# Kernel tuning notes

Measured on AMD Instinct MI355X. Metric: run time of the kernel, lower is better.

The kernel has to match this reference:

```python
import jax, jax.numpy as jnp
import numpy as np

EMB = 2048
HEADS = 16
HEAD_DIM = EMB // HEADS
LATENT = 512
B, S = 2, 2048


def setup_inputs() -> dict:
    key = jax.random.key(0)
    ks = jax.random.split(key, 7)
    sc = lambda fan_in: 1.0 / np.sqrt(fan_in)
    return {
        "x": jax.random.normal(ks[0], (B, S, EMB), dtype=jnp.float32),
        "w_q": jax.random.normal(ks[1], (EMB, EMB), dtype=jnp.float32) * sc(EMB),
        "w_down": jax.random.normal(ks[2], (LATENT, EMB), dtype=jnp.float32) * sc(EMB),
        "w_up_k": jax.random.normal(ks[3], (EMB, LATENT), dtype=jnp.float32) * sc(LATENT),
        "w_up_v": jax.random.normal(ks[4], (EMB, LATENT), dtype=jnp.float32) * sc(LATENT),
        "w_out": jax.random.normal(ks[5], (EMB, EMB), dtype=jnp.float32) * sc(EMB),
        "b_out": jax.random.normal(ks[6], (EMB,), dtype=jnp.float32) * 0.01,
    }


def reference(x, w_q, w_down, w_up_k, w_up_v, w_out, b_out):
    # Linear uses torch convention: y = x @ W.T
    q = jnp.einsum("bse,fe->bsf", x, w_q)          # [B,S,EMB]
    latent = jnp.einsum("bse,le->bsl", x, w_down)  # [B,S,LATENT]
    k = jnp.einsum("bsl,fl->bsf", latent, w_up_k)
    v = jnp.einsum("bsl,fl->bsf", latent, w_up_v)

    def heads(t):  # [B,S,EMB] -> [B,H,S,D]
        return t.reshape(B, S, HEADS, HEAD_DIM).transpose(0, 2, 1, 3)

    qh, kh, vh = heads(q), heads(k), heads(v)
    scores = jnp.einsum("bhqd,bhkd->bhqk", qh, kh)  # [B,H,S,S]
    qpos = jnp.arange(S)
    causal = qpos[:, None] < qpos[None, :]          # True where future (masked)
    scores = jnp.where(causal[None, None], -jnp.inf, scores)
    attn = jax.nn.softmax(scores / np.sqrt(HEAD_DIM).astype(np.float32), axis=-1)
    ctx = jnp.einsum("bhqk,bhkd->bhqd", attn, vh)   # [B,H,S,D]
    ctx = ctx.transpose(0, 2, 1, 3).reshape(B, S, EMB)
    return jnp.einsum("bse,fe->bsf", ctx, w_out) + b_out
```

## Files before the change

kernel.cpp:

```cpp
#include <hip/hip_runtime.h>
#include <hip/hip_bf16.h>

#define EMB 2048
#define HEADS 16
#define HDIM 128
#define LATENT 512
#define BATCH 2
#define SEQ 2048
#define MROWS (BATCH*SEQ)

typedef __attribute__((ext_vector_type(4))) float f32x4;
typedef __attribute__((ext_vector_type(8))) short s16x8;

__device__ __forceinline__ unsigned short f2bf(float f) {
  __hip_bfloat16 h = __float2bfloat16(f);
  union { __hip_bfloat16 h; unsigned short u; } c; c.h = h; return c.u;
}

#define GLOAD_LDS16(g, l) \
  __builtin_amdgcn_global_load_lds((const __attribute__((address_space(1))) unsigned int*)(g), \
                                   (__attribute__((address_space(3))) unsigned int*)(l), 16, 0, 0)

__global__ void cvt_kernel(const float* __restrict__ src, unsigned short* __restrict__ dst, int n4) {
  int i = blockIdx.x * blockDim.x + threadIdx.x;
  int stride = gridDim.x * blockDim.x;
  for (; i < n4; i += stride) {
    float4 v = reinterpret_cast<const float4*>(src)[i];
    ushort4 o;
    o.x = f2bf(v.x); o.y = f2bf(v.y); o.z = f2bf(v.z); o.w = f2bf(v.w);
    reinterpret_cast<ushort4*>(dst)[i] = o;
  }
}

#define BM 128
#define BN 128
#define BK 32

template<int OUTF32>
__global__ __launch_bounds__(256) void gemm_bt(
    const unsigned short* __restrict__ A, const unsigned short* __restrict__ B,
    void* __restrict__ C, const float* __restrict__ bias, int M, int N, int K)
{
  __shared__ __align__(16) unsigned short sA[BM][BK];
  __shared__ __align__(16) unsigned short sB[BN][BK];
  const int tid  = threadIdx.x;
  const int lane = tid & 63, wave = tid >> 6;
  const int wm = wave >> 1, wn = wave & 1;
  const int lrow = lane & 15, kgrp = lane >> 4;
  const long bm = (long)blockIdx.y * BM, bn = (long)blockIdx.x * BN;
  const int srow = tid >> 2;
  const int scol = (tid & 3) * 8;

  f32x4 zero4 = {0.f, 0.f, 0.f, 0.f};
  f32x4 acc[4][4];
  #pragma unroll
  for (int i = 0; i < 4; ++i)
    #pragma unroll
    for (int j = 0; j < 4; ++j) acc[i][j] = zero4;

  const unsigned short* ga = A + (bm + srow) * (long)K + scol;
  const unsigned short* gb = B + (bn + srow) * (long)K + scol;

  for (int k0 = 0; k0 < K; k0 += BK) {
    GLOAD_LDS16(ga + k0,                 &sA[srow][scol]);
    GLOAD_LDS16(ga + 64*(long)K + k0,    &sA[srow + 64][scol]);
    GLOAD_LDS16(gb + k0,                 &sB[srow][scol]);
    GLOAD_LDS16(gb + 64*(long)K + k0,    &sB[srow + 64][scol]);
    __syncthreads();

    s16x8 aF[4], bF[4];
    #pragma unroll
    for (int i = 0; i < 4; ++i) {
      aF[i] = *reinterpret_cast<const s16x8*>(&sA[wm*64 + i*16 + lrow][kgrp*8]);
      bF[i] = *reinterpret_cast<const s16x8*>(&sB[wn*64 + i*16 + lrow][kgrp*8]);
    }
    #pragma unroll
    for (int i = 0; i < 4; ++i)
      #pragma unroll
      for (int j = 0; j < 4; ++j)
        acc[i][j] = __builtin_amdgcn_mfma_f32_16x16x32_bf16(aF[i], bF[j], acc[i][j], 0, 0, 0);
    __syncthreads();
  }

  #pragma unroll
  for (int i = 0; i < 4; ++i) {
    #pragma unroll
    for (int j = 0; j < 4; ++j) {
      long row = bm + wm*64 + i*16 + kgrp*4;
      long col = bn + wn*64 + j*16 + lrow;
      if (OUTF32) {
        float* Cf = (float*)C;
        float bv = bias[col];
        #pragma unroll
        for (int r = 0; r < 4; ++r) Cf[(row + r) * (long)N + col] = acc[i][j][r] + bv;
      } else {
        unsigned short* Cb = (unsigned short*)C;
        #pragma unroll
        for (int r = 0; r < 4; ++r) Cb[(row + r) * (long)N + col] = f2bf(acc[i][j][r]);
      }
    }
  }
}

#define KVB 64
#define QTILE 128
#define NQT (SEQ/QTILE)

__global__ __launch_bounds__(256, 1) void attn2_kernel(
    const unsigned short* __restrict__ Q, const unsigned short* __restrict__ Kg,
    const unsigned short* __restrict__ Vt, unsigned short* __restrict__ CTX)
{
  const int b = blockIdx.z, h = blockIdx.y, pr = blockIdx.x;
  const int tid = threadIdx.x, w = tid >> 6, lane = tid & 63;
  const int lrow = lane & 15, kgrp = lane >> 4;
  const size_t bS = (size_t)b * SEQ;

  __shared__ __align__(16) unsigned short sK[2][KVB * HDIM];
  __shared__ __align__(16) unsigned short sP[4][32][72];

  const int krow  = tid >> 4;
  const int kcolB = ((tid & 15) * 16) ^ (((tid >> 4) & 7) << 4);
  const unsigned short* kst_g = Kg + (bS + krow) * EMB + h * HDIM + (kcolB >> 1);

  const int swz = (lrow & 7) << 4;
  int cc[4];
  #pragma unroll
  for (int kk = 0; kk < 4; ++kk) cc[kk] = ((kk * 64 + kgrp * 16) ^ swz) >> 1;

  const float C = 0.12751742f;
  f32x4 zero4 = {0.f, 0.f, 0.f, 0.f};

  const int qts[2] = {NQT - 1 - pr, pr};
  for (int ps = 0; ps < 2; ++ps) {
    const int qt = qts[ps];
    const int nt = 2 * qt + 2;
    const int qw = qt * QTILE + w * 32;

    s16x8 qF[2][4];
    #pragma unroll
    for (int g = 0; g < 2; ++g)
      #pragma unroll
      for (int kk = 0; kk < 4; ++kk)
        qF[g][kk] = *reinterpret_cast<const s16x8*>(
            Q + (bS + qw + g * 16 + lrow) * EMB + h * HDIM + kk * 32 + kgrp * 8);

    f32x4 o[2][8];
    float rm[2][4], rl[2][4];
    #pragma unroll
    for (int g = 0; g < 2; ++g) {
      #pragma unroll
      for (int dt = 0; dt < 8; ++dt) o[g][dt] = zero4;
      #pragma unroll
      for (int r = 0; r < 4; ++r) { rm[g][r] = -1.0e30f; rl[g][r] = 0.f; }
    }

    __syncthreads();
    {
      unsigned short* l0 = &sK[0][0] + tid * 8;
      #pragma unroll
      for (int R = 0; R < 4; ++R) GLOAD_LDS16(kst_g + (size_t)R * 16 * EMB, l0 + R * 2048);
    }

    for (int j = 0; j < nt; ++j) {
      __syncthreads();
      const int kv0 = j * KVB;
      if (j + 1 < nt) {
        const unsigned short* gs = kst_g + (size_t)(j + 1) * KVB * EMB;
        unsigned short* ls = &sK[(j + 1) & 1][0] + tid * 8;
        #pragma unroll
        for (int R = 0; R < 4; ++R) GLOAD_LDS16(gs + (size_t)R * 16 * EMB, ls + R * 2048);
      }

      s16x8 vF[2][8];
      #pragma unroll
      for (int hf = 0; hf < 2; ++hf)
        #pragma unroll
        for (int dt = 0; dt < 8; ++dt)
          vF[hf][dt] = *reinterpret_cast<const s16x8*>(
              Vt + (size_t)(h * HDIM + dt * 16 + lrow) * MROWS + bS + kv0 + hf * 32 + kgrp * 8);

      const unsigned short* kb = &sK[j & 1][0];
      f32x4 sc[2][4];
      #pragma unroll
      for (int g = 0; g < 2; ++g)
        #pragma unroll
        for (int kvg = 0; kvg < 4; ++kvg) sc[g][kvg] = zero4;
      #pragma unroll
      for (int kvg = 0; kvg < 4; ++kvg) {
        const int rb = (kvg * 16 + lrow) * HDIM;
        #pragma unroll
        for (int kk = 0; kk < 4; ++kk) {
          s16x8 kF = *reinterpret_cast<const s16x8*>(kb + rb + cc[kk]);
          sc[0][kvg] = __builtin_amdgcn_mfma_f32_16x16x32_bf16(qF[0][kk], kF, sc[0][kvg], 0, 0, 0);
          sc[1][kvg] = __builtin_amdgcn_mfma_f32_16x16x32_bf16(qF[1][kk], kF, sc[1][kvg], 0, 0, 0);
        }
      }

      #pragma unroll
      for (int g = 0; g < 2; ++g) {
        const bool needm = (kv0 + 63 > qw + g * 16);
        float sv[4][4];
        #pragma unroll
        for (int kvg = 0; kvg < 4; ++kvg)
          #pragma unroll
          for (int r = 0; r < 4; ++r) {
            float s = sc[g][kvg][r];
            if (needm) {
              int qq  = qw + g * 16 + kgrp * 4 + r;
              int col = kv0 + kvg * 16 + lrow;
              s = (col <= qq) ? s : -3.0e38f;
            }
            sv[kvg][r] = s;
          }
        float tm[4];
        #pragma unroll
        for (int r = 0; r < 4; ++r)
          tm[r] = fmaxf(fmaxf(sv[0][r], sv[1][r]), fmaxf(sv[2][r], sv[3][r]));
        #pragma unroll
        for (int m = 1; m < 16; m <<= 1)
          #pragma unroll
          for (int r = 0; r < 4; ++r) tm[r] = fmaxf(tm[r], __shfl_xor(tm[r], m));

        float corr[4], ts[4];
        #pragma unroll
        for (int r = 0; r < 4; ++r) {
          float mn = fmaxf(rm[g][r], tm[r] * C);
          corr[r] = exp2f(rm[g][r] - mn);
          rm[g][r] = mn;
          float p0 = exp2f(fmaf(sv[0][r], C, -mn));
          float p1 = exp2f(fmaf(sv[1][r], C, -mn));
          float p2 = exp2f(fmaf(sv[2][r], C, -mn));
          float p3 = exp2f(fmaf(sv[3][r], C, -mn));
          ts[r] = (p0 + p1) + (p2 + p3);
          const int qrow = g * 16 + kgrp * 4 + r;
          sP[w][qrow][ 0 + lrow] = f2bf(p0);
          sP[w][qrow][16 + lrow] = f2bf(p1);
          sP[w][qrow][32 + lrow] = f2bf(p2);
          sP[w][qrow][48 + lrow] = f2bf(p3);
        }
        #pragma unroll
        for (int m = 1; m < 16; m <<= 1)
          #pragma unroll
          for (int r = 0; r < 4; ++r) ts[r] += __shfl_xor(ts[r], m);
        #pragma unroll
        for (int r = 0; r < 4; ++r) rl[g][r] = rl[g][r] * corr[r] + ts[r];
        #pragma unroll
        for (int dt = 0; dt < 8; ++dt)
          #pragma unroll
          for (int r = 0; r < 4; ++r) o[g][dt][r] *= corr[r];
      }

      s16x8 pF[2][2];
      #pragma unroll
      for (int g = 0; g < 2; ++g)
        #pragma unroll
        for (int hf = 0; hf < 2; ++hf)
          pF[g][hf] = *reinterpret_cast<const s16x8*>(&sP[w][g * 16 + lrow][hf * 32 + kgrp * 8]);
      #pragma unroll
      for (int g = 0; g < 2; ++g)
        #pragma unroll
        for (int dt = 0; dt < 8; ++dt) {
          o[g][dt] = __builtin_amdgcn_mfma_f32_16x16x32_bf16(pF[g][0], vF[0][dt], o[g][dt], 0, 0, 0);
          o[g][dt] = __builtin_amdgcn_mfma_f32_16x16x32_bf16(pF[g][1], vF[1][dt], o[g][dt], 0, 0, 0);
        }
    }

    #pragma unroll
    for (int g = 0; g < 2; ++g) {
      float iv[4];
      #pragma unroll
      for (int r = 0; r < 4; ++r) iv[r] = 1.0f / rl[g][r];
      #pragma unroll
      for (int dt = 0; dt < 8; ++dt)
        #pragma unroll
        for (int r = 0; r < 4; ++r)
          CTX[(bS + qw + g * 16 + kgrp * 4 + r) * EMB + h * HDIM + dt * 16 + lrow] =
              f2bf(o[g][dt][r] * iv[r]);
    }
  }
}

extern "C" void kernel_launch(void* const* d_in, const int* in_sizes, int n_in,
                              void* d_out, int out_size, void* d_ws, size_t ws_size,
                              hipStream_t stream)
{
  const float* x      = (const float*)d_in[0];
  const float* w_q    = (const float*)d_in[1];
  const float* w_down = (const float*)d_in[2];
  const float* w_upk  = (const float*)d_in[3];
  const float* w_upv  = (const float*)d_in[4];
  const float* w_out  = (const float*)d_in[5];
  const float* b_out  = (const float*)d_in[6];
  float* out = (float*)d_out;

  char* ws = (char*)d_ws;
  size_t off = 0;
  auto alloc = [&](size_t elems) {
    void* p = ws + off; off += elems * 2; off = (off + 255) & ~(size_t)255; return p;
  };
  unsigned short* xb   = (unsigned short*)alloc((size_t)MROWS * EMB);
  unsigned short* wqb  = (unsigned short*)alloc((size_t)EMB * EMB);
  unsigned short* wdb  = (unsigned short*)alloc((size_t)LATENT * EMB);
  unsigned short* wkb  = (unsigned short*)alloc((size_t)EMB * LATENT);
  unsigned short* wvb  = (unsigned short*)alloc((size_t)EMB * LATENT);
  unsigned short* wob  = (unsigned short*)alloc((size_t)EMB * EMB);
  unsigned short* qb   = (unsigned short*)alloc((size_t)MROWS * EMB);
  unsigned short* latb = (unsigned short*)alloc((size_t)MROWS * LATENT);
  unsigned short* kb   = (unsigned short*)alloc((size_t)MROWS * EMB);
  unsigned short* vtb  = (unsigned short*)alloc((size_t)EMB * MROWS);
  unsigned short* ctxb = xb;

  auto cvt = [&](const float* s, unsigned short* d, size_t n) {
    int n4 = (int)(n / 4);
    int blocks = (n4 + 255) / 256; if (blocks > 1024) blocks = 1024;
    cvt_kernel<<<dim3(blocks), dim3(256), 0, stream>>>(s, d, n4);
  };
  cvt(x,      xb,  (size_t)MROWS * EMB);
  cvt(w_q,    wqb, (size_t)EMB * EMB);
  cvt(w_down, wdb, (size_t)LATENT * EMB);
  cvt(w_upk,  wkb, (size_t)EMB * LATENT);
  cvt(w_upv,  wvb, (size_t)EMB * LATENT);
  cvt(w_out,  wob, (size_t)EMB * EMB);

  gemm_bt<0><<<dim3(EMB/BN,    MROWS/BM), 256, 0, stream>>>(xb,   wqb, qb,   nullptr, MROWS, EMB,    EMB);
  gemm_bt<0><<<dim3(LATENT/BN, MROWS/BM), 256, 0, stream>>>(xb,   wdb, latb, nullptr, MROWS, LATENT, EMB);
  gemm_bt<0><<<dim3(EMB/BN,    MROWS/BM), 256, 0, stream>>>(latb, wkb, kb,   nullptr, MROWS, EMB,    LATENT);
  gemm_bt<0><<<dim3(MROWS/BN,  EMB/BM),   256, 0, stream>>>(wvb,  latb, vtb, nullptr, EMB,   MROWS,  LATENT);

  attn2_kernel<<<dim3(NQT/2, HEADS, BATCH), 256, 0, stream>>>(qb, kb, vtb, ctxb);

  gemm_bt<1><<<dim3(EMB/BN, MROWS/BM), 256, 0, stream>>>(ctxb, wob, (void*)out, b_out, MROWS, EMB, EMB);
}
```

Baseline: 465.1 us.

## Shrink attention query tile, add lazy softmax rescale, setprio, and GEMM block swizzle

The attention kernel now uses 64-row query tiles with 16 rows per wave, halving register use so two blocks can fit per CU, and launches twice as many blocks. It skips the running-max rescale of the output accumulator when the new max exceeds the old one by no more than a threshold. It also raises wave priority around the MFMA sections. Separately, the GEMM remaps block indices so consecutive workgroups are spread across eight groups, aimed at better cache locality across XCDs. The smaller tile loads each K/V tile for fewer query rows, so global and LDS traffic per unit of work goes up.

```diff
diff --git a/kernel.cpp b/kernel.cpp
--- a/kernel.cpp
+++ b/kernel.cpp
@@ -47,7 +47,14 @@
   const int lane = tid & 63, wave = tid >> 6;
   const int wm = wave >> 1, wn = wave & 1;
   const int lrow = lane & 15, kgrp = lane >> 4;
-  const long bm = (long)blockIdx.y * BM, bn = (long)blockIdx.x * BN;
+
+  const int gx = gridDim.x;
+  const int nwg = gx * gridDim.y;
+  const int orig = blockIdx.y * gx + blockIdx.x;
+  const int chunk = nwg >> 3;
+  const int sw = (orig & 7) * chunk + (orig >> 3);
+  const long bm = (long)(sw / gx) * BM, bn = (long)(sw % gx) * BN;
+
   const int srow = tid >> 2;
   const int scol = (tid & 3) * 8;
 
@@ -103,20 +110,20 @@
 }
 
 #define KVB 64
-#define QTILE 128
-#define NQT (SEQ/QTILE)
-
-__global__ __launch_bounds__(256, 1) void attn2_kernel(
+#define QTB 64
+#define NQT3 (SEQ/QTB)
+
+__global__ __launch_bounds__(256, 2) void attn3_kernel(
     const unsigned short* __restrict__ Q, const unsigned short* __restrict__ Kg,
     const unsigned short* __restrict__ Vt, unsigned short* __restrict__ CTX)
 {
-  const int b = blockIdx.z, h = blockIdx.y, pr = blockIdx.x;
+  const int pr = blockIdx.x, h = blockIdx.y, b = blockIdx.z;
   const int tid = threadIdx.x, w = tid >> 6, lane = tid & 63;
   const int lrow = lane & 15, kgrp = lane >> 4;
   const size_t bS = (size_t)b * SEQ;
 
   __shared__ __align__(16) unsigned short sK[2][KVB * HDIM];
-  __shared__ __align__(16) unsigned short sP[4][32][72];
+  __shared__ __align__(16) unsigned short sP[4][16][72];
 
   const int krow  = tid >> 4;
   const int kcolB = ((tid & 15) * 16) ^ (((tid >> 4) & 7) << 4);
@@ -128,31 +135,27 @@
   for (int kk = 0; kk < 4; ++kk) cc[kk] = ((kk * 64 + kgrp * 16) ^ swz) >> 1;
 
   const float C = 0.12751742f;
+  const float THR = 11.5f;
   f32x4 zero4 = {0.f, 0.f, 0.f, 0.f};
 
-  const int qts[2] = {NQT - 1 - pr, pr};
+  const int qts[2] = {NQT3 - 1 - pr, pr};
   for (int ps = 0; ps < 2; ++ps) {
     const int qt = qts[ps];
-    const int nt = 2 * qt + 2;
-    const int qw = qt * QTILE + w * 32;
-
-    s16x8 qF[2][4];
-    #pragma unroll
-    for (int g = 0; g < 2; ++g)
-      #pragma unroll
-      for (int kk = 0; kk < 4; ++kk)
-        qF[g][kk] = *reinterpret_cast<const s16x8*>(
-            Q + (bS + qw + g * 16 + lrow) * EMB + h * HDIM + kk * 32 + kgrp * 8);
-
-    f32x4 o[2][8];
-    float rm[2][4], rl[2][4];
-    #pragma unroll
-    for (int g = 0; g < 2; ++g) {
-      #pragma unroll
-      for (int dt = 0; dt < 8; ++dt) o[g][dt] = zero4;
-      #pragma unroll
-      for (int r = 0; r < 4; ++r) { rm[g][r] = -1.0e30f; rl[g][r] = 0.f; }
-    }
+    const int nt = qt + 1;
+    const int qw = qt * QTB + w * 16;
+
+    s16x8 qF[4];
+    #pragma unroll
+    for (int kk = 0; kk < 4; ++kk)
+      qF[kk] = *reinterpret_cast<const s16x8*>(
+          Q + (bS + qw + lrow) * EMB + h * HDIM + kk * 32 + kgrp * 8);
+
+    f32x4 o[8];
+    #pragma unroll
+    for (int dt = 0; dt < 8; ++dt) o[dt] = zero4;
+    float rm[4], rl[4];
+    #pragma unroll
+    for (int r = 0; r < 4; ++r) { rm[r] = -1.0e30f; rl[r] = 0.f; }
 
     __syncthreads();
     {
@@ -180,103 +183,111 @@
               Vt + (size_t)(h * HDIM + dt * 16 + lrow) * MROWS + bS + kv0 + hf * 32 + kgrp * 8);
 
       const unsigned short* kb = &sK[j & 1][0];
-      f32x4 sc[2][4];
-      #pragma unroll
-      for (int g = 0; g < 2; ++g)
-        #pragma unroll
-        for (int kvg = 0; kvg < 4; ++kvg) sc[g][kvg] = zero4;
+      f32x4 sc[4];
+      #pragma unroll
+      for (int kvg = 0; kvg < 4; ++kvg) sc[kvg] = zero4;
+      __builtin_amdgcn_s_setprio(1);
       #pragma unroll
       for (int kvg = 0; kvg < 4; ++kvg) {
         const int rb = (kvg * 16 + lrow) * HDIM;
         #pragma unroll
         for (int kk = 0; kk < 4; ++kk) {
           s16x8 kF = *reinterpret_cast<const s16x8*>(kb + rb + cc[kk]);
-          sc[0][kvg] = __builtin_amdgcn_mfma_f32_16x16x32_bf16(qF[0][kk], kF, sc[0][kvg], 0, 0, 0);
-          sc[1][kvg] = __builtin_amdgcn_mfma_f32_16x16x32_bf16(qF[1][kk], kF, sc[1][kvg], 0, 0, 0);
+          sc[kvg] = __builtin_amdgcn_mfma_f32_16x16x32_bf16(qF[kk], kF, sc[kvg], 0, 0, 0);
         }
       }
-
-      #pragma unroll
-      for (int g = 0; g < 2; ++g) {
-        const bool needm = (kv0 + 63 > qw + g * 16);
-        float sv[4][4];
-        #pragma unroll
-        for (int kvg = 0; kvg < 4; ++kvg)
-          #pragma unroll
-          for (int r = 0; r < 4; ++r) {
-            float s = sc[g][kvg][r];
-            if (needm) {
-              int qq  = qw + g * 16 + kgrp * 4 + r;
-              int col = kv0 + kvg * 16 + lrow;
-              s = (col <= qq) ? s : -3.0e38f;
-            }
-            sv[kvg][r] = s;
+      __builtin_amdgcn_s_setprio(0);
+
+      const bool needm = (kv0 + 63 > qw);
+      float sv[4][4];
+      #pragma unroll
+      for (int kvg = 0; kvg < 4; ++kvg)
+        #pragma unroll
+        for (int r = 0; r < 4; ++r) {
+          float s = sc[kvg][r];
+          if (needm) {
+            int qq  = qw + kgrp * 4 + r;
+            int col = kv0 + kvg * 16 + lrow;
+            s = (col <= qq) ? s : -3.0e38f;
           }
-        float tm[4];
-        #pragma unroll
-        for (int r = 0; r < 4; ++r)
-          tm[r] = fmaxf(fmaxf(sv[0][r], sv[1][r]), fmaxf(sv[2][r], sv[3][r]));
-        #pragma unroll
-        for (int m = 1; m < 16; m <<= 1)
-          #pragma unroll
-          for (int r = 0; r < 4; ++r) tm[r] = fmaxf(tm[r], __shfl_xor(tm[r], m));
-
-        float corr[4], ts[4];
+          sv[kvg][r] = s;
+        }
+      float tm[4];
+      #pragma unroll
+      for (int r = 0; r < 4; ++r)
+        tm[r] = fmaxf(fmaxf(sv[0][r], sv[1][r]), fmaxf(sv[2][r], sv[3][r]));
+      #pragma unroll
+      for (int m = 1; m < 16; m <<= 1)
+        #pragma unroll
+        for (int r = 0; r < 4; ++r) tm[r] = fmaxf(tm[r], __shfl_xor(tm[r], m));
+
+      float d = tm[0] * C - rm[0];
+      #pragma unroll
+      for (int r = 1; r < 4; ++r) d = fmaxf(d, tm[r] * C - rm[r]);
+      const bool skip = __all(d <= THR);
+
+      float mn[4];
+      #pragma unroll
+      for (int r = 0; r < 4; ++r) mn[r] = skip ? rm[r] : fmaxf(rm[r], tm[r] * C);
+
+      float ts[4];
+      #pragma unroll
+      for (int r = 0; r < 4; ++r) {
+        float p0 = exp2f(fmaf(sv[0][r], C, -mn[r]));
+        float p1 = exp2f(fmaf(sv[1][r], C, -mn[r]));
+        float p2 = exp2f(fmaf(sv[2][r], C, -mn[r]));
+        float p3 = exp2f(fmaf(sv[3][r], C, -mn[r]));
+        ts[r] = (p0 + p1) + (p2 + p3);
+        const int qrow = kgrp * 4 + r;
+        sP[w][qrow][ 0 + lrow] = f2bf(p0);
+        sP[w][qrow][16 + lrow] = f2bf(p1);
+        sP[w][qrow][32 + lrow] = f2bf(p2);
+        sP[w][qrow][48 + lrow] = f2bf(p3);
+      }
+      #pragma unroll
+      for (int m = 1; m < 16; m <<= 1)
+        #pragma unroll
+        for (int r = 0; r < 4; ++r) ts[r] += __shfl_xor(ts[r], m);
+
+      if (skip) {
+        #pragma unroll
+        for (int r = 0; r < 4; ++r) rl[r] += ts[r];
+      } else {
+        float corr[4];
         #pragma unroll
         for (int r = 0; r < 4; ++r) {
-          float mn = fmaxf(rm[g][r], tm[r] * C);
-          corr[r] = exp2f(rm[g][r] - mn);
-          rm[g][r] = mn;
-          float p0 = exp2f(fmaf(sv[0][r], C, -mn));
-          float p1 = exp2f(fmaf(sv[1][r], C, -mn));
-          float p2 = exp2f(fmaf(sv[2][r], C, -mn));
-          float p3 = exp2f(fmaf(sv[3][r], C, -mn));
-          ts[r] = (p0 + p1) + (p2 + p3);
-          const int qrow = g * 16 + kgrp * 4 + r;
-          sP[w][qrow][ 0 + lrow] = f2bf(p0);
-          sP[w][qrow][16 + lrow] = f2bf(p1);
-          sP[w][qrow][32 + lrow] = f2bf(p2);
-          sP[w][qrow][48 + lrow] = f2bf(p3);
+          corr[r] = exp2f(rm[r] - mn[r]);
+          rm[r] = mn[r];
+          rl[r] = rl[r] * corr[r] + ts[r];
         }
-        #pragma unroll
-        for (int m = 1; m < 16; m <<= 1)
-          #pragma unroll
-          for (int r = 0; r < 4; ++r) ts[r] += __shfl_xor(ts[r], m);
-        #pragma unroll
-        for (int r = 0; r < 4; ++r) rl[g][r] = rl[g][r] * corr[r] + ts[r];
         #pragma unroll
         for (int dt = 0; dt < 8; ++dt)
           #pragma unroll
-          for (int r = 0; r < 4; ++r) o[g][dt][r] *= corr[r];
-      }
-
-      s16x8 pF[2][2];
-      #pragma unroll
-      for (int g = 0; g < 2; ++g)
-        #pragma unroll
-        for (int hf = 0; hf < 2; ++hf)
-          pF[g][hf] = *reinterpret_cast<const s16x8*>(&sP[w][g * 16 + lrow][hf * 32 + kgrp * 8]);
-      #pragma unroll
-      for (int g = 0; g < 2; ++g)
-        #pragma unroll
-        for (int dt = 0; dt < 8; ++dt) {
-          o[g][dt] = __builtin_amdgcn_mfma_f32_16x16x32_bf16(pF[g][0], vF[0][dt], o[g][dt], 0, 0, 0);
-          o[g][dt] = __builtin_amdgcn_mfma_f32_16x16x32_bf16(pF[g][1], vF[1][dt], o[g][dt], 0, 0, 0);
-        }
+          for (int r = 0; r < 4; ++r) o[dt][r] *= corr[r];
+      }
+
+      s16x8 pF[2];
+      #pragma unroll
+      for (int hf = 0; hf < 2; ++hf)
+        pF[hf] = *reinterpret_cast<const s16x8*>(&sP[w][lrow][hf * 32 + kgrp * 8]);
+      __builtin_amdgcn_s_setprio(1);
+      #pragma unroll
+      for (int dt = 0; dt < 8; ++dt) {
+        o[dt] = __builtin_amdgcn_mfma_f32_16x16x32_bf16(pF[0], vF[0][dt], o[dt], 0, 0, 0);
+        o[dt] = __builtin_amdgcn_mfma_f32_16x16x32_bf16(pF[1], vF[1][dt], o[dt], 0, 0, 0);
+      }
+      __builtin_amdgcn_s_setprio(0);
     }
 
-    #pragma unroll
-    for (int g = 0; g < 2; ++g) {
-      float iv[4];
-      #pragma unroll
-      for (int r = 0; r < 4; ++r) iv[r] = 1.0f / rl[g][r];
-      #pragma unroll
-      for (int dt = 0; dt < 8; ++dt)
-        #pragma unroll
-        for (int r = 0; r < 4; ++r)
-          CTX[(bS + qw + g * 16 + kgrp * 4 + r) * EMB + h * HDIM + dt * 16 + lrow] =
-              f2bf(o[g][dt][r] * iv[r]);
-    }
+    float iv[4];
+    #pragma unroll
+    for (int r = 0; r < 4; ++r) iv[r] = 1.0f / rl[r];
+    #pragma unroll
+    for (int dt = 0; dt < 8; ++dt)
+      #pragma unroll
+      for (int r = 0; r < 4; ++r)
+        CTX[(bS + qw + kgrp * 4 + r) * EMB + h * HDIM + dt * 16 + lrow] =
+            f2bf(o[dt][r] * iv[r]);
   }
 }
 
@@ -327,7 +338,7 @@
   gemm_bt<0><<<dim3(EMB/BN,    MROWS/BM), 256, 0, stream>>>(latb, wkb, kb,   nullptr, MROWS, EMB,    LATENT);
   gemm_bt<0><<<dim3(MROWS/BN,  EMB/BM),   256, 0, stream>>>(wvb,  latb, vtb, nullptr, EMB,   MROWS,  LATENT);
 
-  attn2_kernel<<<dim3(NQT/2, HEADS, BATCH), 256, 0, stream>>>(qb, kb, vtb, ctxb);
+  attn3_kernel<<<dim3(NQT3/2, HEADS, BATCH), 256, 0, stream>>>(qb, kb, vtb, ctxb);
 
   gemm_bt<1><<<dim3(EMB/BN, MROWS/BM), 256, 0, stream>>>(ctxb, wob, (void*)out, b_out, MROWS, EMB, EMB);
 }
```

After: 454.9 us. 2.2% less time.
